# Kernel optimization log

Measured on AMD Instinct MI355X. Metric: run time of the kernel, lower is better.

Reference implementation:

```python
import jax, jax.numpy as jnp
import numpy as np

D_MODEL = 1024
NHEAD = 16
D_FF = 4096
SEQ = 2048
BATCH = 2
EPS = 1e-5


def _layernorm(x, g, b):
    mu = jnp.mean(x, axis=-1, keepdims=True)
    var = jnp.var(x, axis=-1, keepdims=True)
    return (x - mu) * jax.lax.rsqrt(var + EPS) * g + b


def setup_inputs() -> dict:
    key = jax.random.key(0)
    ks = jax.random.split(key, 16)
    s = 0.02
    def lin(k, din, dout):
        return jax.random.normal(k, (din, dout), jnp.float32) * s
    return {
        "x": jax.random.normal(ks[0], (SEQ, BATCH, D_MODEL), jnp.float32),
        "Wq": lin(ks[1], D_MODEL, D_MODEL), "bq": jnp.zeros((D_MODEL,), jnp.float32),
        "Wk": lin(ks[2], D_MODEL, D_MODEL), "bk": jnp.zeros((D_MODEL,), jnp.float32),
        "Wv": lin(ks[3], D_MODEL, D_MODEL), "bv": jnp.zeros((D_MODEL,), jnp.float32),
        "Wo": lin(ks[4], D_MODEL, D_MODEL), "bo": jnp.zeros((D_MODEL,), jnp.float32),
        "W1": lin(ks[5], D_MODEL, D_FF), "b1": jnp.zeros((D_FF,), jnp.float32),
        "W2": lin(ks[6], D_FF, D_MODEL), "b2": jnp.zeros((D_MODEL,), jnp.float32),
        "g1": jnp.ones((D_MODEL,), jnp.float32), "be1": jnp.zeros((D_MODEL,), jnp.float32),
        "g2": jnp.ones((D_MODEL,), jnp.float32), "be2": jnp.zeros((D_MODEL,), jnp.float32),
    }


def reference(x, Wq, bq, Wk, bk, Wv, bv, Wo, bo, W1, b1, W2, b2, g1, be1, g2, be2):
    # batch_first=False: x is [S, B, D] -> [B, S, D]
    xb = jnp.transpose(x, (1, 0, 2))
    B, S, D = xb.shape
    H, Dh = NHEAD, D // NHEAD

    Q = (xb @ Wq + bq).reshape(B, S, H, Dh)
    K = (xb @ Wk + bk).reshape(B, S, H, Dh)
    V = (xb @ Wv + bv).reshape(B, S, H, Dh)

    scores = jnp.einsum('bqhd,bkhd->bhqk', Q, K) / jnp.sqrt(jnp.float32(Dh))
    attn = jax.nn.softmax(scores, axis=-1)
    ctx = jnp.einsum('bhqk,bkhd->bqhd', attn, V).reshape(B, S, D)

    x_att = ctx @ Wo + bo
    xb = xb + x_att
    xb = _layernorm(xb, g1, be1)  # post-norm (norm_first=False)

    h = jax.nn.gelu(xb @ W1 + b1, approximate=False)
    xb = xb + (h @ W2 + b2)
    xb = _layernorm(xb, g2, be2)

    return jnp.transpose(xb, (1, 0, 2))  # back to [S, B, D]
```

## Files before the change

### kernel.cpp

```cpp
#include <hip/hip_runtime.h>
#include <hip/hip_bf16.h>
#include <cstdint>
#include <cstddef>

#define S_LEN 2048
#define BATCHN 2
#define DMODEL 1024
#define NHEADS 16
#define DHEAD 64
#define DFF 4096
#define NTOK (S_LEN*BATCHN)

typedef __bf16 bf16x8 __attribute__((ext_vector_type(8)));
typedef float f32x4 __attribute__((ext_vector_type(4)));
typedef __hip_bfloat16 bf16s;

__device__ static inline void gload_lds16(const void* g, void* l) {
  __builtin_amdgcn_global_load_lds((const __attribute__((address_space(1))) void*)g,
                                   (__attribute__((address_space(3))) void*)l,
                                   16, 0, 0);
}


__global__ __launch_bounds__(256) void transpose_convert(const float* __restrict__ in,
                                                         bf16s* __restrict__ out,
                                                         int K, int N) {
  __shared__ float tile[32][33];
  const int tx = threadIdx.x & 31;
  const int ty = threadIdx.x >> 5;
  const int bx = blockIdx.x * 32;
  const int by = blockIdx.y * 32;
#pragma unroll
  for (int i = 0; i < 32; i += 8)
    tile[ty + i][tx] = in[(size_t)(by + ty + i) * N + bx + tx];
  __syncthreads();
#pragma unroll
  for (int i = 0; i < 32; i += 8)
    out[(size_t)(bx + ty + i) * K + by + tx] = __float2bfloat16(tile[tx][ty + i]);
}

__global__ __launch_bounds__(256) void cvt_bf16_kernel(const float* __restrict__ in,
                                                       bf16s* __restrict__ out, int n4) {
  int i = blockIdx.x * 256 + threadIdx.x;
  if (i < n4) {
    float4 v = ((const float4*)in)[i];
    union { bf16s h[4]; uint2 u; } pk;
    pk.h[0] = __float2bfloat16(v.x); pk.h[1] = __float2bfloat16(v.y);
    pk.h[2] = __float2bfloat16(v.z); pk.h[3] = __float2bfloat16(v.w);
    ((uint2*)out)[i] = pk.u;
  }
}

__global__ __launch_bounds__(256) void bias_concat_kernel(const float* __restrict__ bq,
                                                          const float* __restrict__ bk,
                                                          const float* __restrict__ bv,
                                                          float* __restrict__ bqkv) {
  int i = blockIdx.x * 256 + threadIdx.x;
  if (i < 3 * DMODEL) {
    float v = (i < DMODEL) ? bq[i] : (i < 2 * DMODEL ? bk[i - DMODEL] : bv[i - 2 * DMODEL]);
    bqkv[i] = v;
  }
}

template<int EPI>
__global__ __launch_bounds__(256, 2)
void gemm_kernel(const bf16s* __restrict__ A, const bf16s* __restrict__ Bt,
                 int M, int N, int K,
                 const float* __restrict__ bias,
                 const float* __restrict__ residF,
                 const bf16s* __restrict__ residB,
                 float* __restrict__ outF, bf16s* __restrict__ outB,
                 bf16s* __restrict__ Qb, bf16s* __restrict__ Kb, bf16s* __restrict__ Vtb)
{
  __shared__ bf16s smem[2][2 * 128 * 64];
  const int tid = threadIdx.x;
  const int l = tid & 63;
  const int w = tid >> 6;
  const int m0 = blockIdx.y * 128;
  const int n0 = blockIdx.x * 128;
  const int lr = l & 15, lg = l >> 4;

  f32x4 acc[4][4] = {};

  auto stageAB = [&](int buf, int kt) {
#pragma unroll
    for (int it = 0; it < 4; ++it) {
      int c = it * 4 + w;
      int off = c * 1024 + l * 16;
      int row = off >> 7;
      int kb = (off & 127) ^ ((row & 7) << 4);
      const char* srcA = (const char*)A + ((size_t)(m0 + row) * K + kt) * 2 + kb;
      gload_lds16(srcA, (char*)&smem[buf][0] + c * 1024);
      const char* srcB = (const char*)Bt + ((size_t)(n0 + row) * K + kt) * 2 + kb;
      gload_lds16(srcB, (char*)&smem[buf][0] + 16384 + c * 1024);
    }
  };

  auto compute = [&](int buf) {
    const char* base = (const char*)&smem[buf][0];
    const int wm = (w >> 1) * 64, wn = (w & 1) * 64;
#pragma unroll
    for (int kk = 0; kk < 2; ++kk) {
      bf16x8 af[4], bfr[4];
#pragma unroll
      for (int mi = 0; mi < 4; ++mi) {
        int row = wm + mi * 16 + lr;
        int kb = (kk * 64 + lg * 16) ^ ((row & 7) << 4);
        af[mi] = *(const bf16x8*)(base + row * 128 + kb);
      }
#pragma unroll
      for (int ni = 0; ni < 4; ++ni) {
        int row = wn + ni * 16 + lr;
        int kb = (kk * 64 + lg * 16) ^ ((row & 7) << 4);
        bfr[ni] = *(const bf16x8*)(base + 16384 + row * 128 + kb);
      }
#pragma unroll
      for (int mi = 0; mi < 4; ++mi)
#pragma unroll
        for (int ni = 0; ni < 4; ++ni)
          acc[mi][ni] = __builtin_amdgcn_mfma_f32_16x16x32_bf16(af[mi], bfr[ni], acc[mi][ni], 0, 0, 0);
    }
  };

  const int nt = K / 64;
  stageAB(0, 0);
  __syncthreads();
  int cur = 0;
  for (int t = 0; t < nt - 1; ++t) {
    stageAB(cur ^ 1, (t + 1) * 64);
    compute(cur);
    __syncthreads();
    cur ^= 1;
  }
  compute(cur);

  const int wm = (w >> 1) * 64, wn = (w & 1) * 64;
#pragma unroll
  for (int mi = 0; mi < 4; ++mi) {
#pragma unroll
    for (int ni = 0; ni < 4; ++ni) {
#pragma unroll
      for (int r = 0; r < 4; ++r) {
        int row = m0 + wm + mi * 16 + lg * 4 + r;
        int col = n0 + wn + ni * 16 + lr;
        float v = acc[mi][ni][r] + bias[col];
        if (EPI == 0) {
          int which = col >> 10;
          int h = (col & 1023) >> 6;
          int d = col & 63;
          int b = row & 1;
          int s = row >> 1;
          if (which == 0)
            Qb[(((size_t)(b * NHEADS + h)) * S_LEN + s) * DHEAD + d] = __float2bfloat16(v * 0.125f);
          else if (which == 1)
            Kb[(((size_t)(b * NHEADS + h)) * S_LEN + s) * DHEAD + d] = __float2bfloat16(v);
          else
            Vtb[(((size_t)(b * NHEADS + h)) * DHEAD + d) * S_LEN + s] = __float2bfloat16(v);
        } else if (EPI == 1) {
          outF[(size_t)row * N + col] = v + residF[(size_t)row * N + col];
        } else if (EPI == 2) {
          float gv = 0.5f * v * (1.0f + erff(v * 0.70710678118654752f));
          outB[(size_t)row * N + col] = __float2bfloat16(gv);
        } else {
          outF[(size_t)row * N + col] = v + __bfloat162float(residB[(size_t)row * N + col]);
        }
      }
    }
  }
}

__global__ __launch_bounds__(256)
void attn_kernel(const bf16s* __restrict__ Qb, const bf16s* __restrict__ Kb,
                 const bf16s* __restrict__ Vtb, bf16s* __restrict__ ctx)
{
  __shared__ bf16s Ks[64 * 72];
  __shared__ bf16s Vs[64 * 72];
  __shared__ bf16s Ps[4 * 16 * 72];
  const int tid = threadIdx.x;
  const int l = tid & 63, w = tid >> 6;
  const int qb = blockIdx.x, h = blockIdx.y, b = blockIdx.z;
  const bf16s* Qh = Qb + ((size_t)(b * NHEADS + h)) * S_LEN * DHEAD;
  const bf16s* Kh = Kb + ((size_t)(b * NHEADS + h)) * S_LEN * DHEAD;
  const bf16s* Vh = Vtb + ((size_t)(b * NHEADS + h)) * DHEAD * S_LEN;
  const int lr = l & 15, lg = l >> 4;
  const int qrow = qb * 64 + w * 16 + lr;

  bf16x8 aq[2];
  aq[0] = *(const bf16x8*)(Qh + (size_t)qrow * DHEAD + lg * 8);
  aq[1] = *(const bf16x8*)(Qh + (size_t)qrow * DHEAD + 32 + lg * 8);

  f32x4 o[4] = {};
  float m_run[4] = {-1e30f, -1e30f, -1e30f, -1e30f};
  float l_run[4] = {0.f, 0.f, 0.f, 0.f};

  for (int kt = 0; kt < S_LEN / 64; ++kt) {
    const int s0 = kt * 64;
#pragma unroll
    for (int i = 0; i < 2; ++i) {
      int c = tid + i * 256;
      int row = c >> 3;
      int cb = (c & 7) * 16;
      *(uint4*)((char*)Ks + row * 144 + cb) =
          *(const uint4*)((const char*)Kh + ((size_t)(s0 + row)) * 128 + cb);
      *(uint4*)((char*)Vs + row * 144 + cb) =
          *(const uint4*)((const char*)Vh + (size_t)row * S_LEN * 2 + s0 * 2 + cb);
    }
    __syncthreads();

    f32x4 sc[4] = {};
#pragma unroll
    for (int kk = 0; kk < 2; ++kk) {
#pragma unroll
      for (int ni = 0; ni < 4; ++ni) {
        bf16x8 bk = *(const bf16x8*)((char*)Ks + (ni * 16 + lr) * 144 + kk * 64 + lg * 16);
        sc[ni] = __builtin_amdgcn_mfma_f32_16x16x32_bf16(aq[kk], bk, sc[ni], 0, 0, 0);
      }
    }

    float alpha[4];
#pragma unroll
    for (int r = 0; r < 4; ++r) {
      float mx = fmaxf(fmaxf(sc[0][r], sc[1][r]), fmaxf(sc[2][r], sc[3][r]));
      mx = fmaxf(mx, __shfl_xor(mx, 1));
      mx = fmaxf(mx, __shfl_xor(mx, 2));
      mx = fmaxf(mx, __shfl_xor(mx, 4));
      mx = fmaxf(mx, __shfl_xor(mx, 8));
      float nm = fmaxf(m_run[r], mx);
      alpha[r] = __expf(m_run[r] - nm);
      m_run[r] = nm;
      float rs = 0.f;
#pragma unroll
      for (int ni = 0; ni < 4; ++ni) {
        float p = __expf(sc[ni][r] - nm);
        sc[ni][r] = p;
        rs += p;
      }
      rs += __shfl_xor(rs, 1);
      rs += __shfl_xor(rs, 2);
      rs += __shfl_xor(rs, 4);
      rs += __shfl_xor(rs, 8);
      l_run[r] = l_run[r] * alpha[r] + rs;
#pragma unroll
      for (int di = 0; di < 4; ++di) o[di][r] *= alpha[r];
    }

    char* Pw = (char*)Ps + w * 16 * 144;
#pragma unroll
    for (int ni = 0; ni < 4; ++ni)
#pragma unroll
      for (int r = 0; r < 4; ++r)
        *(bf16s*)(Pw + (lg * 4 + r) * 144 + (ni * 16 + lr) * 2) = __float2bfloat16(sc[ni][r]);

#pragma unroll
    for (int kk = 0; kk < 2; ++kk) {
      bf16x8 ap = *(const bf16x8*)(Pw + lr * 144 + kk * 64 + lg * 16);
#pragma unroll
      for (int di = 0; di < 4; ++di) {
        bf16x8 bv = *(const bf16x8*)((char*)Vs + (di * 16 + lr) * 144 + kk * 64 + lg * 16);
        o[di] = __builtin_amdgcn_mfma_f32_16x16x32_bf16(ap, bv, o[di], 0, 0, 0);
      }
    }
    __syncthreads();
  }

#pragma unroll
  for (int r = 0; r < 4; ++r) {
    float inv = 1.0f / l_run[r];
    int s = qb * 64 + w * 16 + lg * 4 + r;
    int t = s * BATCHN + b;
#pragma unroll
    for (int di = 0; di < 4; ++di) {
      int d = h * DHEAD + di * 16 + lr;
      ctx[(size_t)t * DMODEL + d] = __float2bfloat16(o[di][r] * inv);
    }
  }
}

template<int OUTBF>
__global__ __launch_bounds__(256)
void ln_kernel(const float* __restrict__ in, const float* __restrict__ g,
               const float* __restrict__ be, float* __restrict__ outF,
               bf16s* __restrict__ outB)
{
  const int row = blockIdx.x;
  const int tid = threadIdx.x;
  const float* x = in + (size_t)row * DMODEL;
  float4 v = ((const float4*)x)[tid];
  float s = v.x + v.y + v.z + v.w;
  float s2 = v.x * v.x + v.y * v.y + v.z * v.z + v.w * v.w;
#pragma unroll
  for (int m = 1; m < 64; m <<= 1) { s += __shfl_xor(s, m); s2 += __shfl_xor(s2, m); }
  __shared__ float sm[8];
  const int wv = tid >> 6, l = tid & 63;
  if (l == 0) { sm[wv] = s; sm[4 + wv] = s2; }
  __syncthreads();
  s = sm[0] + sm[1] + sm[2] + sm[3];
  s2 = sm[4] + sm[5] + sm[6] + sm[7];
  float mean = s * (1.0f / DMODEL);
  float var = s2 * (1.0f / DMODEL) - mean * mean;
  float rstd = rsqrtf(var + 1e-5f);
  float4 gv = ((const float4*)g)[tid];
  float4 bv = ((const float4*)be)[tid];
  float o0 = (v.x - mean) * rstd * gv.x + bv.x;
  float o1 = (v.y - mean) * rstd * gv.y + bv.y;
  float o2 = (v.z - mean) * rstd * gv.z + bv.z;
  float o3 = (v.w - mean) * rstd * gv.w + bv.w;
  if (OUTBF) {
    union { bf16s h[4]; uint2 u; } pk;
    pk.h[0] = __float2bfloat16(o0); pk.h[1] = __float2bfloat16(o1);
    pk.h[2] = __float2bfloat16(o2); pk.h[3] = __float2bfloat16(o3);
    ((uint2*)(outB + (size_t)row * DMODEL))[tid] = pk.u;
  } else {
    float4 ov = {o0, o1, o2, o3};
    ((float4*)(outF + (size_t)row * DMODEL))[tid] = ov;
  }
}

extern "C" void kernel_launch(void* const* d_in, const int* in_sizes, int n_in,
                              void* d_out, int out_size, void* d_ws, size_t ws_size,
                              hipStream_t stream) {
  const float* x  = (const float*)d_in[0];
  const float* Wq = (const float*)d_in[1];
  const float* bq = (const float*)d_in[2];
  const float* Wk = (const float*)d_in[3];
  const float* bk = (const float*)d_in[4];
  const float* Wv = (const float*)d_in[5];
  const float* bv = (const float*)d_in[6];
  const float* Wo = (const float*)d_in[7];
  const float* bo = (const float*)d_in[8];
  const float* W1 = (const float*)d_in[9];
  const float* b1 = (const float*)d_in[10];
  const float* W2 = (const float*)d_in[11];
  const float* b2 = (const float*)d_in[12];
  const float* g1 = (const float*)d_in[13];
  const float* be1 = (const float*)d_in[14];
  const float* g2 = (const float*)d_in[15];
  const float* be2 = (const float*)d_in[16];

  char* ws = (char*)d_ws;
  size_t off = 0;
  auto alloc = [&](size_t bytes) -> void* {
    void* p = ws + off;
    off += (bytes + 255) & ~(size_t)255;
    return p;
  };
  bf16s* Wqkv_t = (bf16s*)alloc((size_t)3 * DMODEL * DMODEL * 2);
  bf16s* Wo_t   = (bf16s*)alloc((size_t)DMODEL * DMODEL * 2);
  bf16s* W1_t   = (bf16s*)alloc((size_t)DFF * DMODEL * 2);
  bf16s* W2_t   = (bf16s*)alloc((size_t)DMODEL * DFF * 2);
  float* bqkv   = (float*)alloc((size_t)3 * DMODEL * 4);
  bf16s* Xb     = (bf16s*)alloc((size_t)NTOK * DMODEL * 2);
  bf16s* Qb     = (bf16s*)alloc((size_t)NTOK * DMODEL * 2);
  bf16s* Kb     = (bf16s*)alloc((size_t)NTOK * DMODEL * 2);
  bf16s* Vtb    = (bf16s*)alloc((size_t)NTOK * DMODEL * 2);
  bf16s* ctx    = (bf16s*)alloc((size_t)NTOK * DMODEL * 2);
  float* s1     = (float*)alloc((size_t)NTOK * DMODEL * 4);
  bf16s* y1     = (bf16s*)alloc((size_t)NTOK * DMODEL * 2);
  bf16s* Hb     = (bf16s*)alloc((size_t)NTOK * DFF * 2);
  if (off > ws_size) return;

  transpose_convert<<<dim3(DMODEL / 32, DMODEL / 32), 256, 0, stream>>>(Wq, Wqkv_t, DMODEL, DMODEL);
  transpose_convert<<<dim3(DMODEL / 32, DMODEL / 32), 256, 0, stream>>>(Wk, Wqkv_t + (size_t)DMODEL * DMODEL, DMODEL, DMODEL);
  transpose_convert<<<dim3(DMODEL / 32, DMODEL / 32), 256, 0, stream>>>(Wv, Wqkv_t + (size_t)2 * DMODEL * DMODEL, DMODEL, DMODEL);
  transpose_convert<<<dim3(DMODEL / 32, DMODEL / 32), 256, 0, stream>>>(Wo, Wo_t, DMODEL, DMODEL);
  transpose_convert<<<dim3(DFF / 32, DMODEL / 32), 256, 0, stream>>>(W1, W1_t, DMODEL, DFF);
  transpose_convert<<<dim3(DMODEL / 32, DFF / 32), 256, 0, stream>>>(W2, W2_t, DFF, DMODEL);
  bias_concat_kernel<<<12, 256, 0, stream>>>(bq, bk, bv, bqkv);
  cvt_bf16_kernel<<<(NTOK * DMODEL / 4 + 255) / 256, 256, 0, stream>>>(x, Xb, NTOK * DMODEL / 4);

  gemm_kernel<0><<<dim3(3 * DMODEL / 128, NTOK / 128), 256, 0, stream>>>(
      Xb, Wqkv_t, NTOK, 3 * DMODEL, DMODEL, bqkv, nullptr, nullptr, nullptr, nullptr, Qb, Kb, Vtb);

  attn_kernel<<<dim3(S_LEN / 64, NHEADS, BATCHN), 256, 0, stream>>>(Qb, Kb, Vtb, ctx);

  gemm_kernel<1><<<dim3(DMODEL / 128, NTOK / 128), 256, 0, stream>>>(
      ctx, Wo_t, NTOK, DMODEL, DMODEL, bo, x, nullptr, s1, nullptr, nullptr, nullptr, nullptr);
  ln_kernel<1><<<NTOK, 256, 0, stream>>>(s1, g1, be1, nullptr, y1);
  gemm_kernel<2><<<dim3(DFF / 128, NTOK / 128), 256, 0, stream>>>(
      y1, W1_t, NTOK, DFF, DMODEL, b1, nullptr, nullptr, nullptr, Hb, nullptr, nullptr, nullptr);
  gemm_kernel<3><<<dim3(DMODEL / 128, NTOK / 128), 256, 0, stream>>>(
      Hb, W2_t, NTOK, DMODEL, DFF, b2, nullptr, y1, s1, nullptr, nullptr, nullptr, nullptr);
  ln_kernel<0><<<NTOK, 256, 0, stream>>>(s1, g2, be2, (float*)d_out, nullptr);
}
```

Baseline: 456.5 us.

## Rewrite attention with double-buffered async LDS loads, exp2 softmax, lazy rescale

The attention kernel now gives each wave 32 query rows (128 per block) and double-buffers K/V tiles into LDS with direct global-to-LDS loads on an XOR-swizzled layout. This overlaps tile loads with compute and avoids bank conflicts. Softmax uses exp2 with log2(e) folded into the Q scale, and the rescale is skipped unless the row max grows by more than a threshold. The scores are computed transposed (K as the A operand), blocks are remapped across XCDs, and launch bounds request 2 blocks per CU. The lazy rescale lets unnormalised values grow up to 2^8 before rescaling; this is exact in the final normalisation, but it shifts bf16 rounding of P.

```diff
diff --git a/kernel.cpp b/kernel.cpp
--- a/kernel.cpp
+++ b/kernel.cpp
@@ -12,8 +12,11 @@
 #define NTOK (S_LEN*BATCHN)
 
 typedef __bf16 bf16x8 __attribute__((ext_vector_type(8)));
+typedef __bf16 bf16x4 __attribute__((ext_vector_type(4)));
 typedef float f32x4 __attribute__((ext_vector_type(4)));
 typedef __hip_bfloat16 bf16s;
+
+#define QSCALE 0.18033688011112042592f
 
 __device__ static inline void gload_lds16(const void* g, void* l) {
   __builtin_amdgcn_global_load_lds((const __attribute__((address_space(1))) void*)g,
@@ -151,7 +154,7 @@
           int b = row & 1;
           int s = row >> 1;
           if (which == 0)
-            Qb[(((size_t)(b * NHEADS + h)) * S_LEN + s) * DHEAD + d] = __float2bfloat16(v * 0.125f);
+            Qb[(((size_t)(b * NHEADS + h)) * S_LEN + s) * DHEAD + d] = __float2bfloat16(v * QSCALE);
           else if (which == 1)
             Kb[(((size_t)(b * NHEADS + h)) * S_LEN + s) * DHEAD + d] = __float2bfloat16(v);
           else
@@ -169,109 +172,166 @@
   }
 }
 
-__global__ __launch_bounds__(256)
+__global__ __launch_bounds__(256, 2)
 void attn_kernel(const bf16s* __restrict__ Qb, const bf16s* __restrict__ Kb,
                  const bf16s* __restrict__ Vtb, bf16s* __restrict__ ctx)
 {
-  __shared__ bf16s Ks[64 * 72];
-  __shared__ bf16s Vs[64 * 72];
-  __shared__ bf16s Ps[4 * 16 * 72];
+  __shared__ __align__(1024) char lds[51200];
   const int tid = threadIdx.x;
   const int l = tid & 63, w = tid >> 6;
-  const int qb = blockIdx.x, h = blockIdx.y, b = blockIdx.z;
-  const bf16s* Qh = Qb + ((size_t)(b * NHEADS + h)) * S_LEN * DHEAD;
-  const bf16s* Kh = Kb + ((size_t)(b * NHEADS + h)) * S_LEN * DHEAD;
-  const bf16s* Vh = Vtb + ((size_t)(b * NHEADS + h)) * DHEAD * S_LEN;
   const int lr = l & 15, lg = l >> 4;
-  const int qrow = qb * 64 + w * 16 + lr;
-
-  bf16x8 aq[2];
-  aq[0] = *(const bf16x8*)(Qh + (size_t)qrow * DHEAD + lg * 8);
-  aq[1] = *(const bf16x8*)(Qh + (size_t)qrow * DHEAD + 32 + lg * 8);
-
-  f32x4 o[4] = {};
-  float m_run[4] = {-1e30f, -1e30f, -1e30f, -1e30f};
-  float l_run[4] = {0.f, 0.f, 0.f, 0.f};
-
-  for (int kt = 0; kt < S_LEN / 64; ++kt) {
-    const int s0 = kt * 64;
+
+  int lin = blockIdx.x;
+  int wg = (lin & 7) * 64 + (lin >> 3);
+  int qb = wg & 15;
+  int hb = wg >> 4;
+  int h = hb & 15, b = hb >> 4;
+
+  const char* Qg = (const char*)(Qb + ((size_t)(b * NHEADS + h)) * S_LEN * DHEAD);
+  const char* Kg = (const char*)(Kb + ((size_t)(b * NHEADS + h)) * S_LEN * DHEAD);
+  const char* Vg = (const char*)(Vtb + ((size_t)(b * NHEADS + h)) * DHEAD * S_LEN);
+
+  const int swz = (lr & 7) << 4;
+  const int aK0 = lr * 128 + ((lg * 16) ^ swz);
+  const int aK1 = lr * 128 + ((64 + lg * 16) ^ swz);
+  const int klane = (l >> 3) * 128  + (((l & 7) * 16) ^ ((l & 56) << 1));
+  const int vlane = (l >> 3) * 4096 + (((l & 7) * 16) ^ ((l & 56) << 1));
+  const int l16 = l * 16;
+  char* Pw = lds + 32768 + w * 4608;
+  const int pwA = lr * 144 + lg * 8;
+  const int prA = lr * 144 + lg * 16;
+
+  const int q0 = qb * 128 + w * 32;
+  bf16x8 aq[2][2];
+#pragma unroll
+  for (int qi = 0; qi < 2; ++qi)
+#pragma unroll
+    for (int kk = 0; kk < 2; ++kk)
+      aq[qi][kk] = *(const bf16x8*)(Qg + (size_t)(q0 + qi * 16 + lr) * 128 + kk * 64 + lg * 16);
+
+  f32x4 o0[4] = {}, o1[4] = {};
+  float m0 = -1e30f, m1 = -1e30f;
+  float ls0 = 0.f, ls1 = 0.f;
+
+  const int NT = S_LEN / 64;
+
+  auto stage = [&](char* dK, int tile) {
+    const char* kbg = Kg + (size_t)tile * 8192;
+    const char* vbg = Vg + (size_t)tile * 128;
+    char* dV = dK + 8192;
 #pragma unroll
     for (int i = 0; i < 2; ++i) {
-      int c = tid + i * 256;
-      int row = c >> 3;
-      int cb = (c & 7) * 16;
-      *(uint4*)((char*)Ks + row * 144 + cb) =
-          *(const uint4*)((const char*)Kh + ((size_t)(s0 + row)) * 128 + cb);
-      *(uint4*)((char*)Vs + row * 144 + cb) =
-          *(const uint4*)((const char*)Vh + (size_t)row * S_LEN * 2 + s0 * 2 + cb);
+      int c = w * 2 + i;
+      gload_lds16(kbg + c * 1024 + klane, dK + c * 1024 + l16);
+      gload_lds16(vbg + (size_t)c * 32768 + vlane, dV + c * 1024 + l16);
     }
-    __syncthreads();
-
-    f32x4 sc[4] = {};
-#pragma unroll
-    for (int kk = 0; kk < 2; ++kk) {
-#pragma unroll
-      for (int ni = 0; ni < 4; ++ni) {
-        bf16x8 bk = *(const bf16x8*)((char*)Ks + (ni * 16 + lr) * 144 + kk * 64 + lg * 16);
-        sc[ni] = __builtin_amdgcn_mfma_f32_16x16x32_bf16(aq[kk], bk, sc[ni], 0, 0, 0);
+  };
+
+  stage(lds, 0);
+  asm volatile("s_waitcnt vmcnt(0)" ::: "memory");
+  __builtin_amdgcn_s_barrier();
+
+#define ATTN_ITER(BUF, t)                                                        \
+  {                                                                              \
+    int nxt = ((t) + 1 < NT) ? (t) + 1 : NT - 1;                                 \
+    stage(lds + ((BUF) ^ 1) * 16384, nxt);                                       \
+    const char* bK = lds + (BUF) * 16384;                                        \
+    const char* bV = bK + 8192;                                                  \
+    f32x4 st0[4], st1[4];                                                        \
+    _Pragma("unroll")                                                            \
+    for (int ni = 0; ni < 4; ++ni) {                                             \
+      bf16x8 k0 = *(const bf16x8*)(bK + ni * 2048 + aK0);                        \
+      bf16x8 k1 = *(const bf16x8*)(bK + ni * 2048 + aK1);                        \
+      f32x4 z = {};                                                              \
+      st0[ni] = __builtin_amdgcn_mfma_f32_16x16x32_bf16(k0, aq[0][0], z, 0, 0, 0);\
+      st0[ni] = __builtin_amdgcn_mfma_f32_16x16x32_bf16(k1, aq[0][1], st0[ni], 0, 0, 0);\
+      st1[ni] = __builtin_amdgcn_mfma_f32_16x16x32_bf16(k0, aq[1][0], z, 0, 0, 0);\
+      st1[ni] = __builtin_amdgcn_mfma_f32_16x16x32_bf16(k1, aq[1][1], st1[ni], 0, 0, 0);\
+    }                                                                            \
+    f32x4 vm0 = st0[0], vm1 = st1[0];                                            \
+    _Pragma("unroll")                                                            \
+    for (int ni = 1; ni < 4; ++ni) {                                             \
+      _Pragma("unroll")                                                          \
+      for (int r = 0; r < 4; ++r) {                                              \
+        vm0[r] = fmaxf(vm0[r], st0[ni][r]);                                      \
+        vm1[r] = fmaxf(vm1[r], st1[ni][r]);                                      \
+      }                                                                          \
+    }                                                                            \
+    float mx0 = fmaxf(fmaxf(vm0[0], vm0[1]), fmaxf(vm0[2], vm0[3]));             \
+    float mx1 = fmaxf(fmaxf(vm1[0], vm1[1]), fmaxf(vm1[2], vm1[3]));             \
+    mx0 = fmaxf(mx0, __shfl_xor(mx0, 16)); mx0 = fmaxf(mx0, __shfl_xor(mx0, 32));\
+    mx1 = fmaxf(mx1, __shfl_xor(mx1, 16)); mx1 = fmaxf(mx1, __shfl_xor(mx1, 32));\
+    if (!__all(mx0 <= m0 + 8.f && mx1 <= m1 + 8.f)) {                            \
+      float nm0 = fmaxf(m0, mx0), nm1 = fmaxf(m1, mx1);                          \
+      float al0 = exp2f(m0 - nm0), al1 = exp2f(m1 - nm1);                        \
+      m0 = nm0; m1 = nm1; ls0 *= al0; ls1 *= al1;                                \
+      _Pragma("unroll")                                                          \
+      for (int r = 0; r < 4; ++r) {                                              \
+        float s0r = __shfl(al0, lg * 4 + r);                                     \
+        float s1r = __shfl(al1, lg * 4 + r);                                     \
+        _Pragma("unroll")                                                        \
+        for (int di = 0; di < 4; ++di) { o0[di][r] *= s0r; o1[di][r] *= s1r; }   \
+      }                                                                          \
+    }                                                                            \
+    f32x4 ac0 = {}, ac1 = {};                                                    \
+    _Pragma("unroll")                                                            \
+    for (int ni = 0; ni < 4; ++ni) {                                             \
+      _Pragma("unroll")                                                          \
+      for (int r = 0; r < 4; ++r) {                                              \
+        st0[ni][r] = exp2f(st0[ni][r] - m0);                                     \
+        st1[ni][r] = exp2f(st1[ni][r] - m1);                                     \
+      }                                                                          \
+      ac0 += st0[ni]; ac1 += st1[ni];                                            \
+    }                                                                            \
+    ls0 += ac0[0] + ac0[1] + ac0[2] + ac0[3];                                    \
+    ls1 += ac1[0] + ac1[1] + ac1[2] + ac1[3];                                    \
+    _Pragma("unroll")                                                            \
+    for (int ni = 0; ni < 4; ++ni) {                                             \
+      bf16x4 p0, p1;                                                             \
+      _Pragma("unroll")                                                          \
+      for (int j = 0; j < 4; ++j) { p0[j] = (__bf16)st0[ni][j]; p1[j] = (__bf16)st1[ni][j]; }\
+      *(bf16x4*)(Pw + pwA + ni * 32) = p0;                                       \
+      *(bf16x4*)(Pw + 2304 + pwA + ni * 32) = p1;                                \
+    }                                                                            \
+    _Pragma("unroll")                                                            \
+    for (int kk = 0; kk < 2; ++kk) {                                             \
+      bf16x8 ap0 = *(const bf16x8*)(Pw + prA + kk * 64);                         \
+      bf16x8 ap1 = *(const bf16x8*)(Pw + 2304 + prA + kk * 64);                  \
+      const int av = kk ? aK1 : aK0;                                             \
+      _Pragma("unroll")                                                          \
+      for (int di = 0; di < 4; ++di) {                                           \
+        bf16x8 vv = *(const bf16x8*)(bV + di * 2048 + av);                       \
+        o0[di] = __builtin_amdgcn_mfma_f32_16x16x32_bf16(ap0, vv, o0[di], 0, 0, 0);\
+        o1[di] = __builtin_amdgcn_mfma_f32_16x16x32_bf16(ap1, vv, o1[di], 0, 0, 0);\
+      }                                                                          \
+    }                                                                            \
+    asm volatile("s_waitcnt vmcnt(0)" ::: "memory");                             \
+    __builtin_amdgcn_s_barrier();                                                \
+  }
+
+  for (int t = 0; t < NT; t += 2) {
+    ATTN_ITER(0, t);
+    ATTN_ITER(1, t + 1);
+  }
+#undef ATTN_ITER
+
+#pragma unroll
+  for (int qi = 0; qi < 2; ++qi) {
+    float ls = qi ? ls1 : ls0;
+    ls += __shfl_xor(ls, 16);
+    ls += __shfl_xor(ls, 32);
+    float inv = 1.0f / ls;
+#pragma unroll
+    for (int r = 0; r < 4; ++r) {
+      float invr = __shfl(inv, lg * 4 + r);
+      int srow = q0 + qi * 16 + lg * 4 + r;
+      int tkn = srow * BATCHN + b;
+#pragma unroll
+      for (int di = 0; di < 4; ++di) {
+        int d = h * DHEAD + di * 16 + lr;
+        float v = (qi ? o1[di][r] : o0[di][r]) * invr;
+        ctx[(size_t)tkn * DMODEL + d] = __float2bfloat16(v);
       }
-    }
-
-    float alpha[4];
-#pragma unroll
-    for (int r = 0; r < 4; ++r) {
-      float mx = fmaxf(fmaxf(sc[0][r], sc[1][r]), fmaxf(sc[2][r], sc[3][r]));
-      mx = fmaxf(mx, __shfl_xor(mx, 1));
-      mx = fmaxf(mx, __shfl_xor(mx, 2));
-      mx = fmaxf(mx, __shfl_xor(mx, 4));
-      mx = fmaxf(mx, __shfl_xor(mx, 8));
-      float nm = fmaxf(m_run[r], mx);
-      alpha[r] = __expf(m_run[r] - nm);
-      m_run[r] = nm;
-      float rs = 0.f;
-#pragma unroll
-      for (int ni = 0; ni < 4; ++ni) {
-        float p = __expf(sc[ni][r] - nm);
-        sc[ni][r] = p;
-        rs += p;
-      }
-      rs += __shfl_xor(rs, 1);
-      rs += __shfl_xor(rs, 2);
-      rs += __shfl_xor(rs, 4);
-      rs += __shfl_xor(rs, 8);
-      l_run[r] = l_run[r] * alpha[r] + rs;
-#pragma unroll
-      for (int di = 0; di < 4; ++di) o[di][r] *= alpha[r];
-    }
-
-    char* Pw = (char*)Ps + w * 16 * 144;
-#pragma unroll
-    for (int ni = 0; ni < 4; ++ni)
-#pragma unroll
-      for (int r = 0; r < 4; ++r)
-        *(bf16s*)(Pw + (lg * 4 + r) * 144 + (ni * 16 + lr) * 2) = __float2bfloat16(sc[ni][r]);
-
-#pragma unroll
-    for (int kk = 0; kk < 2; ++kk) {
-      bf16x8 ap = *(const bf16x8*)(Pw + lr * 144 + kk * 64 + lg * 16);
-#pragma unroll
-      for (int di = 0; di < 4; ++di) {
-        bf16x8 bv = *(const bf16x8*)((char*)Vs + (di * 16 + lr) * 144 + kk * 64 + lg * 16);
-        o[di] = __builtin_amdgcn_mfma_f32_16x16x32_bf16(ap, bv, o[di], 0, 0, 0);
-      }
-    }
-    __syncthreads();
-  }
-
-#pragma unroll
-  for (int r = 0; r < 4; ++r) {
-    float inv = 1.0f / l_run[r];
-    int s = qb * 64 + w * 16 + lg * 4 + r;
-    int t = s * BATCHN + b;
-#pragma unroll
-    for (int di = 0; di < 4; ++di) {
-      int d = h * DHEAD + di * 16 + lr;
-      ctx[(size_t)t * DMODEL + d] = __float2bfloat16(o[di][r] * inv);
     }
   }
 }
@@ -371,7 +431,7 @@
   gemm_kernel<0><<<dim3(3 * DMODEL / 128, NTOK / 128), 256, 0, stream>>>(
       Xb, Wqkv_t, NTOK, 3 * DMODEL, DMODEL, bqkv, nullptr, nullptr, nullptr, nullptr, Qb, Kb, Vtb);
 
-  attn_kernel<<<dim3(S_LEN / 64, NHEADS, BATCHN), 256, 0, stream>>>(Qb, Kb, Vtb, ctx);
+  attn_kernel<<<512, 256, 0, stream>>>(Qb, Kb, Vtb, ctx);
 
   gemm_kernel<1><<<dim3(DMODEL / 128, NTOK / 128), 256, 0, stream>>>(
       ctx, Wo_t, NTOK, DMODEL, DMODEL, bo, x, nullptr, s1, nullptr, nullptr, nullptr, nullptr);
```

Measured after the change: 396.8 us. 13.1% less time.
